# Kernel optimization log

Measured on AMD Instinct MI355X. Metric: run time of the kernel, lower is better.

The kernel has to match this reference:

```python
import jax, jax.numpy as jnp
import numpy as np
import math

B, S, D, H, R = 4, 4096, 1024, 16, 256
DK = D // H

def setup_inputs() -> dict:
    key = jax.random.key(0)
    ks = jax.random.split(key, 16)
    def lin(k, fan_in, fan_out):
        # torch Linear default init: U(-1/sqrt(fan_in), 1/sqrt(fan_in))
        bound = 1.0 / math.sqrt(fan_in)
        kw, kb = jax.random.split(k)
        W = jax.random.uniform(kw, (fan_out, fan_in), jnp.float32, -bound, bound)
        b = jax.random.uniform(kb, (fan_out,), jnp.float32, -bound, bound)
        return W, b
    Wq, bq = lin(ks[0], D, D)
    Wk, bk = lin(ks[1], D, D)
    Wv, bv = lin(ks[2], D, D)
    Wo, bo = lin(ks[3], D, D)
    # xavier_uniform over last two dims (S, R)
    xav = math.sqrt(6.0 / (S + R))
    E = jax.random.uniform(ks[4], (H, S, R), jnp.float32, -xav, xav)
    F = jax.random.uniform(ks[5], (H, S, R), jnp.float32, -xav, xav)
    query = jax.random.normal(ks[6], (B, S, D), jnp.float32)
    key_ = jax.random.normal(ks[7], (B, S, D), jnp.float32)
    value = jax.random.normal(ks[8], (B, S, D), jnp.float32)
    return {"query": query, "key": key_, "value": value,
            "Wq": Wq, "bq": bq, "Wk": Wk, "bk": bk, "Wv": Wv, "bv": bv,
            "Wo": Wo, "bo": bo, "E": E, "F": F}

def _split_heads(x):
    # [B, S, D] -> [B, H, S, DK]
    b, s, _ = x.shape
    return x.reshape(b, s, H, DK).transpose(0, 2, 1, 3)

def reference(query, key, value, Wq, bq, Wk, bk, Wv, bv, Wo, bo, E, F):
    q = _split_heads(query @ Wq.T + bq)   # [B,H,S,DK]
    k = _split_heads(key @ Wk.T + bk)
    v = _split_heads(value @ Wv.T + bv)
    # key^T @ E : [B,H,DK,S] @ [H,S,R] -> [B,H,DK,R]
    kp = jnp.einsum('bhsd,hsr->bhdr', k, E)
    vp = jnp.einsum('bhsd,hsr->bhdr', v, F)
    attn = jnp.einsum('bhsd,bhdr->bhsr', q, kp) / math.sqrt(DK)
    attn = jax.nn.softmax(attn, axis=-1)  # [B,H,S,R]
    out = jnp.einsum('bhsr,bhdr->bhsd', attn, vp)  # [B,H,S,DK]
    out = out.transpose(0, 2, 1, 3).reshape(query.shape[0], -1, D)
    return out @ Wo.T + bo
```

## Files before the change

### kernel.cpp

```cpp
#include <hip/hip_runtime.h>


typedef __bf16 bf16;
typedef bf16 bf16x8 __attribute__((ext_vector_type(8)));
typedef bf16 bf16x4 __attribute__((ext_vector_type(4)));
typedef float f32x4 __attribute__((ext_vector_type(4)));

constexpr int BB = 4, SS = 4096, DD = 1024, HH = 16, RR = 256, DK = 64;

#define QSCALE 0.1803368801111204f

__device__ __forceinline__ void gl2lds16(const void* g, void* l, int lane)
{
#if __has_builtin(__builtin_amdgcn_global_load_lds)
    auto gp = reinterpret_cast<const __attribute__((address_space(1))) void*>(
        reinterpret_cast<uintptr_t>(g));
    auto lp = reinterpret_cast<__attribute__((address_space(3))) void*>(
        reinterpret_cast<uintptr_t>(l));
    __builtin_amdgcn_global_load_lds(gp, lp, 16, 0, 0);
    (void)lane;
#else
    *(bf16x8*)((char*)l + lane * 16) = *(const bf16x8*)g;
#endif
}

#define VMW3  asm volatile("s_waitcnt vmcnt(3)" ::: "memory")
#define VMW0  asm volatile("s_waitcnt vmcnt(0)" ::: "memory")
#define LGKM0 asm volatile("s_waitcnt lgkmcnt(0)" ::: "memory")

__global__ void cvt_f32_bf16(const float* __restrict__ in, bf16* __restrict__ out, int n)
{
    int i = (blockIdx.x * 256 + threadIdx.x) * 8;
    if (i < n) {
        float4 v0 = *(const float4*)(in + i);
        float4 v1 = *(const float4*)(in + i + 4);
        bf16x8 h;
        h[0] = (bf16)v0.x; h[1] = (bf16)v0.y; h[2] = (bf16)v0.z; h[3] = (bf16)v0.w;
        h[4] = (bf16)v1.x; h[5] = (bf16)v1.y; h[6] = (bf16)v1.z; h[7] = (bf16)v1.w;
        *(bf16x8*)(out + i) = h;
    }
}

__global__ void transpose_cvt(const float* __restrict__ in, bf16* __restrict__ out,
                              int rows, int cols)
{
    __shared__ float t[64][65];
    const float* I = in + (size_t)blockIdx.z * rows * cols;
    bf16* O = out + (size_t)blockIdx.z * rows * cols;
    int c0 = blockIdx.x * 64, r0 = blockIdx.y * 64;
    int tx = threadIdx.x, ty = threadIdx.y;
#pragma unroll
    for (int i = ty; i < 64; i += 4)
        t[i][tx] = I[(size_t)(r0 + i) * cols + c0 + tx];
    __syncthreads();
#pragma unroll
    for (int i = ty; i < 64; i += 4)
        O[(size_t)(c0 + i) * rows + r0 + tx] = (bf16)t[tx][i];
}

template <bool OUT_F32>
__global__ __launch_bounds__(512, 4) void gemm_bt(const bf16* __restrict__ A,
                                                  const bf16* __restrict__ W,
                                                  const float* __restrict__ bias,
                                                  void* __restrict__ Cp,
                                                  int M, int N, int K, float oscale)
{
    __shared__ bf16 As[2][256][32];
    __shared__ bf16 Bs[2][128][32];
    const int tid = threadIdx.x, wv = tid >> 6, lane = tid & 63;
    const int g = lane >> 4, lr = lane & 15;

    const int nwg = gridDim.x;
    const int cpx = nwg >> 3;
    const int bid = blockIdx.x;
    const int swz = (bid & 7) * cpx + (bid >> 3);
    const int gx = N >> 7;
    const int mt = swz / gx, nt = swz % gx;
    const int m0 = mt * 256, n0 = nt * 128;
    const int wm = (wv >> 1) * 64, wn = (wv & 1) * 64;

    const int srow = lane >> 2;
    const int scol = ((lane & 3) ^ ((lane >> 4) & 3)) * 8;

    f32x4 acc[4][4] = {};

    auto stageA = [&](int buf, int tk) {
#pragma unroll
        for (int s2 = 0; s2 < 2; ++s2) {
            int c = wv * 2 + s2;
            gl2lds16(A + (size_t)(m0 + c * 16 + srow) * 1024 + tk * 32 + scol,
                     &As[buf][c * 16][0], lane);
        }
    };
    auto stageB = [&](int buf, int tk) {
        gl2lds16(W + (size_t)(n0 + wv * 16 + srow) * 1024 + tk * 32 + scol,
                 &Bs[buf][wv * 16][0], lane);
    };

#define PHK(PB, STAGE_STMT, VM_STMT)                                             \
    {                                                                            \
        const int so = (g ^ (lr >> 2)) << 4;                                     \
        bf16x8 aF[4], bF[4];                                                     \
        _Pragma("unroll") for (int mm = 0; mm < 4; ++mm)                         \
            aF[mm] = *(const bf16x8*)((const char*)&As[PB][wm + mm * 16 + lr][0] + so); \
        _Pragma("unroll") for (int nn = 0; nn < 4; ++nn)                         \
            bF[nn] = *(const bf16x8*)((const char*)&Bs[PB][wn + nn * 16 + lr][0] + so); \
        LGKM0;                                                                   \
        __builtin_amdgcn_s_barrier();                 \
        STAGE_STMT;                                     \
        VM_STMT;                                             \
        __builtin_amdgcn_s_barrier();                   \
        __builtin_amdgcn_sched_barrier(0);                                       \
        __builtin_amdgcn_s_setprio(1);                                           \
        _Pragma("unroll") for (int mm = 0; mm < 4; ++mm) {                       \
            _Pragma("unroll") for (int nn = 0; nn < 4; ++nn) {                   \
                acc[mm][nn] = __builtin_amdgcn_mfma_f32_16x16x32_bf16(           \
                    aF[mm], bF[nn], acc[mm][nn], 0, 0, 0); } }                   \
        __builtin_amdgcn_s_setprio(0);                                           \
    }

    stageA(0, 0); stageB(0, 0);
    stageA(1, 1); stageB(1, 1);
    VMW3;
    __builtin_amdgcn_s_barrier();

#pragma unroll 1
    for (int t = 0; t < 30; ++t) {
        const int pb = t & 1;
        PHK(pb, { stageA(pb, t + 2); stageB(pb, t + 2); }, VMW3);
    }
    PHK(0, (void)0, VMW0);
    PHK(1, (void)0, (void)0);
#undef PHK

    float bv[4];
#pragma unroll
    for (int n = 0; n < 4; ++n) bv[n] = bias[n0 + wn + n * 16 + lr];

    if constexpr (OUT_F32) {
#pragma unroll
        for (int n = 0; n < 4; ++n) {
            int col = n0 + wn + n * 16 + lr;
#pragma unroll
            for (int m = 0; m < 4; ++m) {
                int row = m0 + wm + m * 16 + 4 * g;
#pragma unroll
                for (int i = 0; i < 4; ++i)
                    ((float*)Cp)[(size_t)(row + i) * N + col] = (acc[m][n][i] + bv[n]) * oscale;
            }
        }
    } else {
        char* myb = (char*)&As[0][0][0] + wv * 4096;
#pragma unroll
        for (int mh = 0; mh < 2; ++mh) {
#pragma unroll
            for (int mm = 0; mm < 2; ++mm)
#pragma unroll
                for (int n = 0; n < 4; ++n) {
                    int colb = (n * 16 + lr) * 2;
#pragma unroll
                    for (int i = 0; i < 4; ++i) {
                        int row = mm * 16 + 4 * g + i;
                        *(bf16*)(myb + row * 128 + (colb ^ ((row & 7) << 4))) =
                            (bf16)((acc[mh * 2 + mm][n][i] + bv[n]) * oscale);
                    }
                }
            __builtin_amdgcn_wave_barrier();
            bf16* Cb = (bf16*)Cp + (size_t)(m0 + wm + mh * 32) * N + n0 + wn;
#pragma unroll
            for (int it = 0; it < 4; ++it) {
                int r = it * 8 + (lane >> 3);
                int sl = lane & 7;
                bf16x8 vv = *(const bf16x8*)(myb + r * 128 + ((sl ^ (r & 7)) << 4));
                *(bf16x8*)(Cb + (size_t)r * N + sl * 8) = vv;
            }
            __builtin_amdgcn_wave_barrier();
        }
    }
}

__global__ __launch_bounds__(256) void kpvp_gemm(const bf16* __restrict__ X,
                                                 const float* __restrict__ E,
                                                 float* __restrict__ out)
{
    __shared__ bf16 Ak[64][40];
    const int b = blockIdx.z, h = blockIdx.y;
    const int s0 = blockIdx.x * 512;
    const int tid = threadIdx.x, wv = tid >> 6, lane = tid & 63;
    const int g = lane >> 4, lr = lane & 15;
    const float* Eh = E + (size_t)h * SS * RR;
    const int rbase = wv * 64 + lr;
    f32x4 acc[4][4] = {};

    for (int kt = 0; kt < 512; kt += 32) {
        const int sb = s0 + kt;
        __syncthreads();
        float ef[4][8];
        const float* Eb = Eh + (size_t)(sb + g * 8) * RR + rbase;
#pragma unroll
        for (int n = 0; n < 4; ++n)
#pragma unroll
            for (int j = 0; j < 8; ++j)
                ef[n][j] = Eb[(size_t)j * RR + n * 16];
        {
            int sl = tid >> 3, dblk = (tid & 7) * 8;
            bf16x8 v = *(const bf16x8*)(X + ((size_t)b * SS + sb + sl) * DD + h * DK + dblk);
#pragma unroll
            for (int j = 0; j < 8; ++j) Ak[dblk + j][sl] = v[j];
        }
        bf16x8 bb[4];
#pragma unroll
        for (int n = 0; n < 4; ++n)
#pragma unroll
            for (int j = 0; j < 8; ++j)
                bb[n][j] = (bf16)ef[n][j];
        __syncthreads();

        bf16x8 a[4];
#pragma unroll
        for (int m = 0; m < 4; ++m) a[m] = *(const bf16x8*)&Ak[m * 16 + lr][g * 8];
#pragma unroll
        for (int m = 0; m < 4; ++m)
#pragma unroll
            for (int n = 0; n < 4; ++n)
                acc[m][n] = __builtin_amdgcn_mfma_f32_16x16x32_bf16(a[m], bb[n], acc[m][n], 0, 0, 0);
    }

    float* o = out + ((size_t)(b * HH + h)) * DK * RR;
#pragma unroll
    for (int m = 0; m < 4; ++m)
#pragma unroll
        for (int n = 0; n < 4; ++n) {
            int r = wv * 64 + n * 16 + lr;
#pragma unroll
            for (int i = 0; i < 4; ++i)
                atomicAdd(o + (size_t)(m * 16 + 4 * g + i) * RR + r, acc[m][n][i]);
        }
}

__global__ __launch_bounds__(512) void attn_fused(const bf16* __restrict__ qb,
                                                  const bf16* __restrict__ kpt,
                                                  const bf16* __restrict__ vpb,
                                                  bf16* __restrict__ ctx)
{
    __shared__ bf16 KPs[256][72];
    __shared__ bf16 VPs[64][264];
    __shared__ bf16 Ps[8][16][264];
    const int b = blockIdx.z, h = blockIdx.y, qt = blockIdx.x;
    const int tid = threadIdx.x, wv = tid >> 6, lane = tid & 63;
    const int g = lane >> 4, lr = lane & 15;
    const bf16* kph = kpt + ((size_t)(b * HH + h)) * RR * DK;
    const bf16* vph = vpb + ((size_t)(b * HH + h)) * DK * RR;

#pragma unroll
    for (int p = 0; p < 4; ++p) {
        int f = p * 512 + tid;
        *(bf16x8*)&KPs[f >> 3][(f & 7) * 8] = *(const bf16x8*)(kph + (size_t)f * 8);
        *(bf16x8*)&VPs[f >> 5][(f & 31) * 8] = *(const bf16x8*)(vph + (size_t)f * 8);
    }

    const bf16* qbase = qb + (size_t)b * SS * DD + h * DK;
    int row0 = qt * 1024 + wv * 16;
    bf16x8 aq0 = *(const bf16x8*)(qbase + (size_t)(row0 + lr) * DD + g * 8);
    bf16x8 aq1 = *(const bf16x8*)(qbase + (size_t)(row0 + lr) * DD + 32 + g * 8);
    __syncthreads();

    for (int it = 0; it < 8; ++it) {
        f32x4 acc[16] = {};
        __builtin_amdgcn_s_setprio(1);
#pragma unroll
        for (int nf = 0; nf < 16; ++nf) {
            bf16x8 b0 = *(const bf16x8*)&KPs[nf * 16 + lr][g * 8];
            bf16x8 b1 = *(const bf16x8*)&KPs[nf * 16 + lr][32 + g * 8];
            acc[nf] = __builtin_amdgcn_mfma_f32_16x16x32_bf16(aq0, b0, acc[nf], 0, 0, 0);
            acc[nf] = __builtin_amdgcn_mfma_f32_16x16x32_bf16(aq1, b1, acc[nf], 0, 0, 0);
        }
        __builtin_amdgcn_s_setprio(0);

        bf16x8 aqn0 = aq0, aqn1 = aq1;
        if (it < 7) {
            const bf16* qr = qbase + (size_t)(row0 + 128 + lr) * DD;
            aqn0 = *(const bf16x8*)(qr + g * 8);
            aqn1 = *(const bf16x8*)(qr + 32 + g * 8);
        }

        float rs[4];
#pragma unroll
        for (int i = 0; i < 4; ++i) {
            float s = 0.f;
#pragma unroll
            for (int nf = 0; nf < 16; ++nf) {
                float pv = exp2f(acc[nf][i]);
                acc[nf][i] = pv;
                s += pv;
            }
#pragma unroll
            for (int msk = 1; msk < 16; msk <<= 1) s += __shfl_xor(s, msk, 64);
            rs[i] = 1.f / s;
        }

#pragma unroll
        for (int nf = 0; nf < 16; ++nf)
#pragma unroll
            for (int i = 0; i < 4; ++i)
                Ps[wv][4 * g + i][nf * 16 + lr] = (bf16)acc[nf][i];
        __builtin_amdgcn_wave_barrier();

        f32x4 o[4] = {};
        __builtin_amdgcn_s_setprio(1);
#pragma unroll
        for (int ks = 0; ks < 8; ++ks) {
            bf16x8 pa = *(const bf16x8*)&Ps[wv][lr][ks * 32 + g * 8];
#pragma unroll
            for (int n = 0; n < 4; ++n) {
                bf16x8 vb = *(const bf16x8*)&VPs[n * 16 + lr][ks * 32 + g * 8];
                o[n] = __builtin_amdgcn_mfma_f32_16x16x32_bf16(pa, vb, o[n], 0, 0, 0);
            }
        }
        __builtin_amdgcn_s_setprio(0);
        __builtin_amdgcn_wave_barrier();

#pragma unroll
        for (int n = 0; n < 4; ++n)
#pragma unroll
            for (int i = 0; i < 4; ++i)
                Ps[wv][4 * g + i][n * 16 + lr] = (bf16)(o[n][i] * rs[i]);
        __builtin_amdgcn_wave_barrier();
        bf16* crow = ctx + (size_t)(b * SS + row0) * DD + h * DK;
#pragma unroll
        for (int p = 0; p < 2; ++p) {
            int r = p * 8 + (lane >> 3), c = (lane & 7) * 8;
            bf16x8 ov = *(const bf16x8*)&Ps[wv][r][c];
            *(bf16x8*)(crow + (size_t)r * DD + c) = ov;
        }
        __builtin_amdgcn_wave_barrier();

        aq0 = aqn0; aq1 = aqn1;
        row0 += 128;
    }
}

extern "C" void kernel_launch(void* const* d_in, const int* in_sizes, int n_in,
                              void* d_out, int out_size, void* d_ws, size_t ws_size,
                              hipStream_t stream)
{
    const float* query = (const float*)d_in[0];
    const float* key   = (const float*)d_in[1];
    const float* value = (const float*)d_in[2];
    const float* Wq = (const float*)d_in[3];  const float* bq = (const float*)d_in[4];
    const float* Wk = (const float*)d_in[5];  const float* bk = (const float*)d_in[6];
    const float* Wv = (const float*)d_in[7];  const float* bv = (const float*)d_in[8];
    const float* Wo = (const float*)d_in[9];  const float* bo = (const float*)d_in[10];
    const float* E  = (const float*)d_in[11];
    const float* F  = (const float*)d_in[12];

    char* w = (char*)d_ws;
    size_t off = 0;
    auto alloc = [&](size_t bytes) -> char* {
        char* p = w + off;
        off += (bytes + 255) & ~(size_t)255;
        return p;
    };

    const size_t DW   = (size_t)DD * DD;
    const size_t BSD  = (size_t)BB * SS * DD;
    const size_t BHDR = (size_t)BB * HH * DK * RR;

    bf16* wqb = (bf16*)alloc(DW * 2);
    bf16* wkb = (bf16*)alloc(DW * 2);
    bf16* wvb = (bf16*)alloc(DW * 2);
    bf16* wob = (bf16*)alloc(DW * 2);
    bf16* qin = (bf16*)alloc(BSD * 2);
    bf16* kin = (bf16*)alloc(BSD * 2);
    bf16* vin = (bf16*)alloc(BSD * 2);
    bf16* qbuf = (bf16*)alloc(BSD * 2);
    bf16* kbuf = (bf16*)alloc(BSD * 2);
    bf16* vbuf = (bf16*)alloc(BSD * 2);
    if (off > ws_size) return;

    float* kpf  = (float*)qin;
    float* vpf  = kpf + BHDR;
    bf16*  kpt  = (bf16*)kin;
    bf16*  vpbb = kpt + BHDR;
    bf16*  ctx  = (bf16*)vin;

    cvt_f32_bf16<<<(int)(DW / 2048), 256, 0, stream>>>(Wq, wqb, (int)DW);
    cvt_f32_bf16<<<(int)(DW / 2048), 256, 0, stream>>>(Wk, wkb, (int)DW);
    cvt_f32_bf16<<<(int)(DW / 2048), 256, 0, stream>>>(Wv, wvb, (int)DW);
    cvt_f32_bf16<<<(int)(DW / 2048), 256, 0, stream>>>(Wo, wob, (int)DW);
    cvt_f32_bf16<<<(int)(BSD / 2048), 256, 0, stream>>>(query, qin, (int)BSD);
    cvt_f32_bf16<<<(int)(BSD / 2048), 256, 0, stream>>>(key,   kin, (int)BSD);
    cvt_f32_bf16<<<(int)(BSD / 2048), 256, 0, stream>>>(value, vin, (int)BSD);

    const int nwg = ((BB * SS) / 256) * (DD / 128);
    gemm_bt<false><<<nwg, 512, 0, stream>>>(qin, wqb, bq, qbuf, BB * SS, DD, DD, QSCALE);
    gemm_bt<false><<<nwg, 512, 0, stream>>>(kin, wkb, bk, kbuf, BB * SS, DD, DD, 1.0f);
    gemm_bt<false><<<nwg, 512, 0, stream>>>(vin, wvb, bv, vbuf, BB * SS, DD, DD, 1.0f);

    hipMemsetAsync(kpf, 0, BHDR * 4 * 2, stream);
    kpvp_gemm<<<dim3(SS / 512, HH, BB), 256, 0, stream>>>(kbuf, E, kpf);
    kpvp_gemm<<<dim3(SS / 512, HH, BB), 256, 0, stream>>>(vbuf, F, vpf);

    dim3 tb(64, 4);
    transpose_cvt<<<dim3(RR / 64, DK / 64, BB * HH), tb, 0, stream>>>(kpf, kpt, DK, RR);
    cvt_f32_bf16<<<(int)(BHDR / 2048), 256, 0, stream>>>(vpf, vpbb, (int)BHDR);

    attn_fused<<<dim3(SS / 1024, HH, BB), 512, 0, stream>>>(qbuf, kpt, vpbb, ctx);

    gemm_bt<true><<<nwg, 512, 0, stream>>>(ctx, wob, bo, d_out, BB * SS, DD, DD, 1.0f);
}
```

Baseline: 384.4 us.

## Fuse fp32-to-bf16 input conversion into Q/K/V projection GEMM A-loads

```diff
diff --git a/kernel.cpp b/kernel.cpp
--- a/kernel.cpp
+++ b/kernel.cpp
@@ -24,6 +24,7 @@
 #endif
 }
 
+#define VMW5  asm volatile("s_waitcnt vmcnt(5)" ::: "memory")
 #define VMW3  asm volatile("s_waitcnt vmcnt(3)" ::: "memory")
 #define VMW0  asm volatile("s_waitcnt vmcnt(0)" ::: "memory")
 #define LGKM0 asm volatile("s_waitcnt lgkmcnt(0)" ::: "memory")
@@ -58,11 +59,132 @@
         O[(size_t)(c0 + i) * rows + r0 + tx] = (bf16)t[tx][i];
 }
 
-template <bool OUT_F32>
+__global__ __launch_bounds__(512, 4) void gemm_qkv(const float* __restrict__ A,
+                                                   const bf16* __restrict__ W,
+                                                   const float* __restrict__ bias,
+                                                   bf16* __restrict__ Cp,
+                                                   int M, int N, int K, float oscale)
+{
+    __shared__ bf16 As[2][256][32];
+    __shared__ bf16 Bs[2][128][32];
+    const int tid = threadIdx.x, wv = tid >> 6, lane = tid & 63;
+    const int g = lane >> 4, lr = lane & 15;
+
+    const int nwg = gridDim.x;
+    const int cpx = nwg >> 3;
+    const int bid = blockIdx.x;
+    const int swz = (bid & 7) * cpx + (bid >> 3);
+    const int gx = N >> 7;
+    const int mt = swz / gx, nt = swz % gx;
+    const int m0 = mt * 256, n0 = nt * 128;
+    const int wm = (wv >> 1) * 64, wn = (wv & 1) * 64;
+
+    const int srow = lane >> 2;
+    const int scol = ((lane & 3) ^ ((lane >> 4) & 3)) * 8;
+
+    const int ar = tid >> 1, ah = tid & 1;
+    const int axs = (ar >> 2) & 3;
+    const float* Ag = A + (size_t)(m0 + ar) * 1024 + ah * 16;
+
+    f32x4 acc[4][4] = {};
+    float4 rE[4], rO[4];
+
+    auto issueA = [&](float4* rr, int tk) {
+#pragma unroll
+        for (int ld = 0; ld < 4; ++ld)
+            rr[ld] = *(const float4*)(Ag + tk * 32 + ld * 4);
+    };
+    auto writeA = [&](int buf, const float4* rr) {
+        bf16x8 h0, h1;
+        h0[0] = (bf16)rr[0].x; h0[1] = (bf16)rr[0].y; h0[2] = (bf16)rr[0].z; h0[3] = (bf16)rr[0].w;
+        h0[4] = (bf16)rr[1].x; h0[5] = (bf16)rr[1].y; h0[6] = (bf16)rr[1].z; h0[7] = (bf16)rr[1].w;
+        h1[0] = (bf16)rr[2].x; h1[1] = (bf16)rr[2].y; h1[2] = (bf16)rr[2].z; h1[3] = (bf16)rr[2].w;
+        h1[4] = (bf16)rr[3].x; h1[5] = (bf16)rr[3].y; h1[6] = (bf16)rr[3].z; h1[7] = (bf16)rr[3].w;
+        *(bf16x8*)&As[buf][ar][((ah * 2 + 0) ^ axs) * 8] = h0;
+        *(bf16x8*)&As[buf][ar][((ah * 2 + 1) ^ axs) * 8] = h1;
+    };
+    auto stageB = [&](int buf, int tk) {
+        gl2lds16(W + (size_t)(n0 + wv * 16 + srow) * 1024 + tk * 32 + scol,
+                 &Bs[buf][wv * 16][0], lane);
+    };
+
+#define PHQ(PB, ISSUE_STMT, VM_STMT, WRITE_STMT)                                 \
+    {                                                                            \
+        const int so = (g ^ (lr >> 2)) << 4;                                     \
+        bf16x8 aF[4], bF[4];                                                     \
+        _Pragma("unroll") for (int mm = 0; mm < 4; ++mm)                         \
+            aF[mm] = *(const bf16x8*)((const char*)&As[PB][wm + mm * 16 + lr][0] + so); \
+        _Pragma("unroll") for (int nn = 0; nn < 4; ++nn)                         \
+            bF[nn] = *(const bf16x8*)((const char*)&Bs[PB][wn + nn * 16 + lr][0] + so); \
+        LGKM0;                                                                   \
+        __builtin_amdgcn_s_barrier();                 \
+        ISSUE_STMT;                                 \
+        VM_STMT;                                     \
+        WRITE_STMT;                                     \
+        LGKM0;                                             \
+        __builtin_amdgcn_s_barrier();                      \
+        __builtin_amdgcn_sched_barrier(0);                                       \
+        __builtin_amdgcn_s_setprio(1);                                           \
+        _Pragma("unroll") for (int mm = 0; mm < 4; ++mm) {                       \
+            _Pragma("unroll") for (int nn = 0; nn < 4; ++nn) {                   \
+                acc[mm][nn] = __builtin_amdgcn_mfma_f32_16x16x32_bf16(           \
+                    aF[mm], bF[nn], acc[mm][nn], 0, 0, 0); } }                   \
+        __builtin_amdgcn_s_setprio(0);                                           \
+    }
+
+    issueA(rE, 0); stageB(0, 0);
+    issueA(rO, 1); stageB(1, 1);
+    VMW5;
+    writeA(0, rE);
+    LGKM0;
+    __builtin_amdgcn_s_barrier();
+
+#pragma unroll 1
+    for (int tt = 0; tt < 15; ++tt) {
+        const int t = tt * 2;
+        PHQ(0, { issueA(rE, t + 2); stageB(0, t + 2); }, VMW5, writeA(1, rO));
+        PHQ(1, { issueA(rO, t + 3); stageB(1, t + 3); }, VMW5, writeA(0, rE));
+    }
+    PHQ(0, (void)0, VMW0, writeA(1, rO));
+    PHQ(1, (void)0, (void)0, (void)0);
+#undef PHQ
+
+    float bv[4];
+#pragma unroll
+    for (int n = 0; n < 4; ++n) bv[n] = bias[n0 + wn + n * 16 + lr];
+
+    char* myb = (char*)&As[0][0][0] + wv * 4096;
+#pragma unroll
+    for (int mh = 0; mh < 2; ++mh) {
+#pragma unroll
+        for (int mm = 0; mm < 2; ++mm)
+#pragma unroll
+            for (int n = 0; n < 4; ++n) {
+                int colb = (n * 16 + lr) * 2;
+#pragma unroll
+                for (int i = 0; i < 4; ++i) {
+                    int row = mm * 16 + 4 * g + i;
+                    *(bf16*)(myb + row * 128 + (colb ^ ((row & 7) << 4))) =
+                        (bf16)((acc[mh * 2 + mm][n][i] + bv[n]) * oscale);
+                }
+            }
+        __builtin_amdgcn_wave_barrier();
+        bf16* Cb = Cp + (size_t)(m0 + wm + mh * 32) * N + n0 + wn;
+#pragma unroll
+        for (int it = 0; it < 4; ++it) {
+            int r = it * 8 + (lane >> 3);
+            int sl = lane & 7;
+            bf16x8 vv = *(const bf16x8*)(myb + r * 128 + ((sl ^ (r & 7)) << 4));
+            *(bf16x8*)(Cb + (size_t)r * N + sl * 8) = vv;
+        }
+        __builtin_amdgcn_wave_barrier();
+    }
+}
+
 __global__ __launch_bounds__(512, 4) void gemm_bt(const bf16* __restrict__ A,
                                                   const bf16* __restrict__ W,
                                                   const float* __restrict__ bias,
-                                                  void* __restrict__ Cp,
+                                                  float* __restrict__ Cp,
                                                   int M, int N, int K, float oscale)
 {
     __shared__ bf16 As[2][256][32];
@@ -106,10 +228,10 @@
         _Pragma("unroll") for (int nn = 0; nn < 4; ++nn)                         \
             bF[nn] = *(const bf16x8*)((const char*)&Bs[PB][wn + nn * 16 + lr][0] + so); \
         LGKM0;                                                                   \
-        __builtin_amdgcn_s_barrier();                 \
-        STAGE_STMT;                                     \
-        VM_STMT;                                             \
-        __builtin_amdgcn_s_barrier();                   \
+        __builtin_amdgcn_s_barrier();                                            \
+        STAGE_STMT;                                                              \
+        VM_STMT;                                                                 \
+        __builtin_amdgcn_s_barrier();                                            \
         __builtin_amdgcn_sched_barrier(0);                                       \
         __builtin_amdgcn_s_setprio(1);                                           \
         _Pragma("unroll") for (int mm = 0; mm < 4; ++mm) {                       \
@@ -137,44 +259,15 @@
 #pragma unroll
     for (int n = 0; n < 4; ++n) bv[n] = bias[n0 + wn + n * 16 + lr];
 
-    if constexpr (OUT_F32) {
-#pragma unroll
-        for (int n = 0; n < 4; ++n) {
-            int col = n0 + wn + n * 16 + lr;
-#pragma unroll
-            for (int m = 0; m < 4; ++m) {
-                int row = m0 + wm + m * 16 + 4 * g;
-#pragma unroll
-                for (int i = 0; i < 4; ++i)
-                    ((float*)Cp)[(size_t)(row + i) * N + col] = (acc[m][n][i] + bv[n]) * oscale;
-            }
-        }
-    } else {
-        char* myb = (char*)&As[0][0][0] + wv * 4096;
-#pragma unroll
-        for (int mh = 0; mh < 2; ++mh) {
-#pragma unroll
-            for (int mm = 0; mm < 2; ++mm)
-#pragma unroll
-                for (int n = 0; n < 4; ++n) {
-                    int colb = (n * 16 + lr) * 2;
-#pragma unroll
-                    for (int i = 0; i < 4; ++i) {
-                        int row = mm * 16 + 4 * g + i;
-                        *(bf16*)(myb + row * 128 + (colb ^ ((row & 7) << 4))) =
-                            (bf16)((acc[mh * 2 + mm][n][i] + bv[n]) * oscale);
-                    }
-                }
-            __builtin_amdgcn_wave_barrier();
-            bf16* Cb = (bf16*)Cp + (size_t)(m0 + wm + mh * 32) * N + n0 + wn;
-#pragma unroll
-            for (int it = 0; it < 4; ++it) {
-                int r = it * 8 + (lane >> 3);
-                int sl = lane & 7;
-                bf16x8 vv = *(const bf16x8*)(myb + r * 128 + ((sl ^ (r & 7)) << 4));
-                *(bf16x8*)(Cb + (size_t)r * N + sl * 8) = vv;
-            }
-            __builtin_amdgcn_wave_barrier();
+#pragma unroll
+    for (int n = 0; n < 4; ++n) {
+        int col = n0 + wn + n * 16 + lr;
+#pragma unroll
+        for (int m = 0; m < 4; ++m) {
+            int row = m0 + wm + m * 16 + 4 * g;
+#pragma unroll
+            for (int i = 0; i < 4; ++i)
+                Cp[(size_t)(row + i) * N + col] = (acc[m][n][i] + bv[n]) * oscale;
         }
     }
 }
@@ -370,32 +463,29 @@
     bf16* wkb = (bf16*)alloc(DW * 2);
     bf16* wvb = (bf16*)alloc(DW * 2);
     bf16* wob = (bf16*)alloc(DW * 2);
-    bf16* qin = (bf16*)alloc(BSD * 2);
-    bf16* kin = (bf16*)alloc(BSD * 2);
-    bf16* vin = (bf16*)alloc(BSD * 2);
+    bf16* scr1 = (bf16*)alloc(BSD * 2);
+    bf16* scr2 = (bf16*)alloc(BSD * 2);
+    bf16* scr3 = (bf16*)alloc(BSD * 2);
     bf16* qbuf = (bf16*)alloc(BSD * 2);
     bf16* kbuf = (bf16*)alloc(BSD * 2);
     bf16* vbuf = (bf16*)alloc(BSD * 2);
     if (off > ws_size) return;
 
-    float* kpf  = (float*)qin;
+    float* kpf  = (float*)scr1;
     float* vpf  = kpf + BHDR;
-    bf16*  kpt  = (bf16*)kin;
+    bf16*  kpt  = (bf16*)scr2;
     bf16*  vpbb = kpt + BHDR;
-    bf16*  ctx  = (bf16*)vin;
+    bf16*  ctx  = (bf16*)scr3;
 
     cvt_f32_bf16<<<(int)(DW / 2048), 256, 0, stream>>>(Wq, wqb, (int)DW);
     cvt_f32_bf16<<<(int)(DW / 2048), 256, 0, stream>>>(Wk, wkb, (int)DW);
     cvt_f32_bf16<<<(int)(DW / 2048), 256, 0, stream>>>(Wv, wvb, (int)DW);
     cvt_f32_bf16<<<(int)(DW / 2048), 256, 0, stream>>>(Wo, wob, (int)DW);
-    cvt_f32_bf16<<<(int)(BSD / 2048), 256, 0, stream>>>(query, qin, (int)BSD);
-    cvt_f32_bf16<<<(int)(BSD / 2048), 256, 0, stream>>>(key,   kin, (int)BSD);
-    cvt_f32_bf16<<<(int)(BSD / 2048), 256, 0, stream>>>(value, vin, (int)BSD);
 
     const int nwg = ((BB * SS) / 256) * (DD / 128);
-    gemm_bt<false><<<nwg, 512, 0, stream>>>(qin, wqb, bq, qbuf, BB * SS, DD, DD, QSCALE);
-    gemm_bt<false><<<nwg, 512, 0, stream>>>(kin, wkb, bk, kbuf, BB * SS, DD, DD, 1.0f);
-    gemm_bt<false><<<nwg, 512, 0, stream>>>(vin, wvb, bv, vbuf, BB * SS, DD, DD, 1.0f);
+    gemm_qkv<<<nwg, 512, 0, stream>>>(query, wqb, bq, qbuf, BB * SS, DD, DD, QSCALE);
+    gemm_qkv<<<nwg, 512, 0, stream>>>(key,   wkb, bk, kbuf, BB * SS, DD, DD, 1.0f);
+    gemm_qkv<<<nwg, 512, 0, stream>>>(value, wvb, bv, vbuf, BB * SS, DD, DD, 1.0f);
 
     hipMemsetAsync(kpf, 0, BHDR * 4 * 2, stream);
     kpvp_gemm<<<dim3(SS / 512, HH, BB), 256, 0, stream>>>(kbuf, E, kpf);
@@ -407,5 +497,5 @@
 
     attn_fused<<<dim3(SS / 1024, HH, BB), 512, 0, stream>>>(qbuf, kpt, vpbb, ctx);
 
-    gemm_bt<true><<<nwg, 512, 0, stream>>>(ctx, wob, bo, d_out, BB * SS, DD, DD, 1.0f);
-}
+    gemm_bt<<<nwg, 512, 0, stream>>>(ctx, wob, bo, (float*)d_out, BB * SS, DD, DD, 1.0f);
+}
```

Result: slower. 1.080 ms (+181.0%).

## Double-buffer LDS fragment reads in registers to overlap with MFMA

Applied to the files above, without the earlier changes.

```diff
diff --git a/kernel.cpp b/kernel.cpp
--- a/kernel.cpp
+++ b/kernel.cpp
@@ -59,7 +59,7 @@
 }
 
 template <bool OUT_F32>
-__global__ __launch_bounds__(512, 4) void gemm_bt(const bf16* __restrict__ A,
+__global__ __launch_bounds__(512, 2) void gemm_bt(const bf16* __restrict__ A,
                                                   const bf16* __restrict__ W,
                                                   const float* __restrict__ bias,
                                                   void* __restrict__ Cp,
@@ -81,8 +81,10 @@
 
     const int srow = lane >> 2;
     const int scol = ((lane & 3) ^ ((lane >> 4) & 3)) * 8;
+    const int so = (g ^ (lr >> 2)) << 4;
 
     f32x4 acc[4][4] = {};
+    bf16x8 aX[4], bX[4], aY[4], bY[4];
 
     auto stageA = [&](int buf, int tk) {
 #pragma unroll
@@ -97,41 +99,52 @@
                  &Bs[buf][wv * 16][0], lane);
     };
 
-#define PHK(PB, STAGE_STMT, VM_STMT)                                             \
+#define RD(aS, bS, PB)                                                           \
     {                                                                            \
-        const int so = (g ^ (lr >> 2)) << 4;                                     \
-        bf16x8 aF[4], bF[4];                                                     \
         _Pragma("unroll") for (int mm = 0; mm < 4; ++mm)                         \
-            aF[mm] = *(const bf16x8*)((const char*)&As[PB][wm + mm * 16 + lr][0] + so); \
+            aS[mm] = *(const bf16x8*)((const char*)&As[PB][wm + mm * 16 + lr][0] + so); \
         _Pragma("unroll") for (int nn = 0; nn < 4; ++nn)                         \
-            bF[nn] = *(const bf16x8*)((const char*)&Bs[PB][wn + nn * 16 + lr][0] + so); \
-        LGKM0;                                                                   \
-        __builtin_amdgcn_s_barrier();                 \
-        STAGE_STMT;                                     \
-        VM_STMT;                                             \
-        __builtin_amdgcn_s_barrier();                   \
-        __builtin_amdgcn_sched_barrier(0);                                       \
+            bS[nn] = *(const bf16x8*)((const char*)&Bs[PB][wn + nn * 16 + lr][0] + so); \
+    }
+#define MM(aS, bS)                                                               \
+    {                                                                            \
         __builtin_amdgcn_s_setprio(1);                                           \
         _Pragma("unroll") for (int mm = 0; mm < 4; ++mm) {                       \
             _Pragma("unroll") for (int nn = 0; nn < 4; ++nn) {                   \
                 acc[mm][nn] = __builtin_amdgcn_mfma_f32_16x16x32_bf16(           \
-                    aF[mm], bF[nn], acc[mm][nn], 0, 0, 0); } }                   \
+                    aS[mm], bS[nn], acc[mm][nn], 0, 0, 0); } }                   \
         __builtin_amdgcn_s_setprio(0);                                           \
+    }
+#define PH(CUR_A, CUR_B, NXT_A, NXT_B, PB, STAGE_STMT, VM_STMT)                  \
+    {                                                                            \
+        LGKM0;                                      \
+        __builtin_amdgcn_s_barrier();            \
+        STAGE_STMT;                                      \
+        VM_STMT;                                           \
+        __builtin_amdgcn_s_barrier();                           \
+        __builtin_amdgcn_sched_barrier(0);                                       \
+        RD(NXT_A, NXT_B, PB ^ 1);                \
+        __builtin_amdgcn_sched_barrier(0);                                       \
+        MM(CUR_A, CUR_B);                                                        \
     }
 
     stageA(0, 0); stageB(0, 0);
     stageA(1, 1); stageB(1, 1);
     VMW3;
     __builtin_amdgcn_s_barrier();
+    RD(aX, bX, 0);
 
 #pragma unroll 1
-    for (int t = 0; t < 30; ++t) {
-        const int pb = t & 1;
-        PHK(pb, { stageA(pb, t + 2); stageB(pb, t + 2); }, VMW3);
-    }
-    PHK(0, (void)0, VMW0);
-    PHK(1, (void)0, (void)0);
-#undef PHK
+    for (int t = 0; t < 30; t += 2) {
+        PH(aX, bX, aY, bY, 0, { stageA(0, t + 2); stageB(0, t + 2); }, VMW3);
+        PH(aY, bY, aX, bX, 1, { stageA(1, t + 3); stageB(1, t + 3); }, VMW3);
+    }
+    PH(aX, bX, aY, bY, 0, (void)0, VMW0);
+    LGKM0;
+    MM(aY, bY);
+#undef PH
+#undef MM
+#undef RD
 
     float bv[4];
 #pragma unroll
```

Result: slower. 414.7 us (+7.9%).
